# Optimization experiments

Measured on AMD Instinct MI355X. Metric: run time of the kernel, lower is better.

Reference implementation:

```python
import jax, jax.numpy as jnp
import numpy as np

I1, I2, N = 256, 256, 512
B = 2048
FLAT = (I1 + 1) * (I2 + 1)  # 66049


def setup_inputs() -> dict:
    key = jax.random.key(0)
    k1, k2, k3, k4 = jax.random.split(key, 4)
    s1 = 1.0 / np.sqrt(FLAT)
    s2 = 1.0 / np.sqrt(N)
    return {
        "inp1": jax.random.normal(k1, (B, I1), dtype=jnp.float32),
        "inp2": jax.random.normal(k2, (B, I2), dtype=jnp.float32),
        "W1": jax.random.normal(k3, (FLAT, N), dtype=jnp.float32) * s1,
        "b1": jnp.zeros((N,), dtype=jnp.float32),
        "W2": jax.random.normal(k4, (N, N), dtype=jnp.float32) * s2,
        "b2": jnp.zeros((N,), dtype=jnp.float32),
    }


def reference(inp1, inp2, W1, b1, W2, b2):
    b = inp1.shape[0]
    ones = jnp.ones((b, 1), dtype=inp1.dtype)
    a = jnp.concatenate([inp1, ones], axis=-1)  # [B, I1+1]
    c = jnp.concatenate([inp2, ones], axis=-1)  # [B, I2+1]
    # per-sample outer product, flattened: [B, (I1+1)*(I2+1)]
    fusion = jnp.einsum("bi,bj->bij", a, c).reshape(b, -1)
    h = jax.nn.relu(fusion @ W1 + b1)
    return jax.nn.relu(h @ W2 + b2)
```

## Files before the change

### kernel.cpp

```cpp
#include <hip/hip_runtime.h>
#include <hip/hip_bf16.h>
#include <stdint.h>

#define BATCH 2048
#define NHID  512
#define KMAIN 65792
#define KPAD  66112
#define NSTEP 1033
#define SPLITS 8
#define AW 320
#define CW 256

typedef __attribute__((ext_vector_type(8))) short short8;
typedef __attribute__((ext_vector_type(4))) short short4v;
typedef __attribute__((ext_vector_type(4))) float f32x4;

#define AS1 __attribute__((address_space(1)))
#define AS3 __attribute__((address_space(3)))

__device__ __forceinline__ unsigned short f2bf(float f) {
    union { float f; unsigned int u; } v; v.f = f;
    unsigned int r = v.u + 0x7FFFu + ((v.u >> 16) & 1u);
    return (unsigned short)(r >> 16);
}
__device__ __forceinline__ float bf2f(unsigned short u) {
    union { unsigned int i; float f; } v; v.i = ((unsigned int)u) << 16;
    return v.f;
}

__device__ __forceinline__ int w1_src_row(int k) {
    if (k < KMAIN) return (k >> 8) * 257 + (k & 255);
    int i = k - KMAIN;
    return (i < 257) ? (i * 257 + 256) : -1;
}

__global__ __launch_bounds__(256) void prep_kernel(
        const float* __restrict__ inp1, const float* __restrict__ inp2,
        const float* __restrict__ W1, const float* __restrict__ W2,
        unsigned short* __restrict__ W1t, unsigned short* __restrict__ W2t,
        unsigned short* __restrict__ a_tab, unsigned short* __restrict__ c_tab) {
    __shared__ float T[64][65];
    int b = blockIdx.x;
    int t = threadIdx.x;

    if (b < 8264 + 64) {
        const float* src; unsigned short* dst; int k0, n0, Kpad; bool perm;
        if (b < 8264) {
            int kt = b % 1033, nt = b / 1033;
            src = W1; dst = W1t; k0 = kt * 64; n0 = nt * 64; Kpad = KPAD; perm = true;
        } else {
            int bb = b - 8264;
            int kt = bb & 7, nt = bb >> 3;
            src = W2; dst = W2t; k0 = kt * 64; n0 = nt * 64; Kpad = 512; perm = false;
        }
        int nn = t & 63, kk0 = t >> 6;
#pragma unroll
        for (int it = 0; it < 16; ++it) {
            int kk = it * 4 + kk0;
            int k = k0 + kk;
            int row = perm ? w1_src_row(k) : k;
            float v = (row >= 0) ? src[(long)row * NHID + n0 + nn] : 0.f;
            T[kk][nn] = v;
        }
        __syncthreads();
#pragma unroll
        for (int it = 0; it < 2; ++it) {
            int idx = it * 256 + t;
            int nl = idx >> 3, ch = idx & 7;
            short8 o;
#pragma unroll
            for (int e = 0; e < 8; ++e) o[e] = (short)f2bf(T[ch * 8 + e][nl]);
            *reinterpret_cast<short8*>(&dst[(long)(n0 + nl) * Kpad + k0 + ch * 8]) = o;
        }
    } else {
        int r0 = (b - 8328) * 32;
        for (int idx = t; idx < 32 * (AW / 8); idx += 256) {
            int r = idx / 40, ch = idx - r * 40;
            int m = r0 + r;
            short8 o;
#pragma unroll
            for (int e = 0; e < 8; ++e) {
                int i = ch * 8 + e;
                float v = (i < 256) ? inp1[m * 256 + i] : (i == 256 ? 1.0f : 0.0f);
                o[e] = (short)f2bf(v);
            }
            *reinterpret_cast<short8*>(&a_tab[m * AW + ch * 8]) = o;
        }
        for (int idx = t; idx < 32 * (CW / 8); idx += 256) {
            int r = idx >> 5, ch = idx & 31;
            int m = r0 + r;
            short8 o;
#pragma unroll
            for (int e = 0; e < 8; ++e) o[e] = (short)f2bf(inp2[m * 256 + ch * 8 + e]);
            *reinterpret_cast<short8*>(&c_tab[m * CW + ch * 8]) = o;
        }
    }
}

__device__ __forceinline__ void stage_tile128(const unsigned short* __restrict__ g,
        long row0, long k0, long ld, unsigned short* lds) {
    int t = threadIdx.x;
    int wave = t >> 6, lane = t & 63;
    int rl = lane >> 3;
    int ch = (lane & 7) ^ rl;
    const unsigned short* src0 = g + (row0 + wave * 8 + rl) * ld + k0 + ch * 8;
#pragma unroll
    for (int r = 0; r < 4; ++r) {
        const unsigned short* src = src0 + (long)r * 32 * ld;
        unsigned short* dst = lds + (r * 32 + wave * 8) * 64;
        __builtin_amdgcn_global_load_lds((const AS1 unsigned int*)src,
                                         (AS3 unsigned int*)dst, 16, 0, 0);
    }
}

__device__ __forceinline__ short8 read_frag(const unsigned short* lds,
        int rowbase, int kofs, int lane) {
    int row = rowbase + (lane & 15);
    int chunkL = (kofs >> 3) + (lane >> 4);
    int sw = chunkL ^ (row & 7);
    return *reinterpret_cast<const short8*>(&lds[row * 64 + sw * 8]);
}

__global__ __launch_bounds__(256, 2) void gemm1_kernel(
        const unsigned short* __restrict__ a_tab,
        const unsigned short* __restrict__ c_tab,
        const unsigned short* __restrict__ W1t, float* __restrict__ hacc) {
    __shared__ __align__(16) unsigned short B_s[3 * 128 * 64];
    __shared__ __align__(16) unsigned short a_lds[128 * 40];

    int bid = (blockIdx.x & 7) * 64 + (blockIdx.x >> 3);
    int m0 = (bid & 15) * 128;
    int n0 = ((bid >> 4) & 3) * 128;
    int s  = bid >> 6;
    int st0 = s * 128;
    int stLast = st0 + 127;

    int lane = threadIdx.x & 63;
    int wv = threadIdx.x >> 6;
    int lrow = wv * 32 + (lane & 15);
    int rowA0g = m0 + lrow;
    int rowA1g = rowA0g + 16;
    int kq = (lane >> 4) * 8;
    int r4 = (lane >> 4) * 4;
    int abase = wv * 32 + r4;

    short8 cc0[8], cc1[8];
#pragma unroll
    for (int q = 0; q < 8; ++q) {
        cc0[q] = *reinterpret_cast<const short8*>(&c_tab[rowA0g * CW + kq + q * 32]);
        cc1[q] = *reinterpret_cast<const short8*>(&c_tab[rowA1g * CW + kq + q * 32]);
    }
    for (int u = threadIdx.x; u < 512; u += 256) {
        int r = u >> 2, chk = u & 3;
        short8 v = *reinterpret_cast<const short8*>(&a_tab[(m0 + r) * AW + s * 32 + chk * 8]);
        *reinterpret_cast<short8*>(&a_lds[r * 40 + chk * 8]) = v;
    }

    f32x4 acc[2][8];
#pragma unroll
    for (int a = 0; a < 2; ++a)
#pragma unroll
        for (int b = 0; b < 8; ++b) acc[a][b] = (f32x4){0.f, 0.f, 0.f, 0.f};

    stage_tile128(W1t, n0, (long)st0 * 64, KPAD, B_s);
    stage_tile128(W1t, n0, (long)(st0 + 1) * 64, KPAD, B_s + 8192);
    __syncthreads();

    int cur = 0;
    for (int g = 0; g < 32; ++g) {
        f32x4 P[2][8];
#pragma unroll
        for (int a = 0; a < 2; ++a)
#pragma unroll
            for (int b = 0; b < 8; ++b) P[a][b] = (f32x4){0.f, 0.f, 0.f, 0.f};
#pragma unroll
        for (int p = 0; p < 4; ++p) {
            int st = st0 + g * 4 + p;
            if (st == stLast) asm volatile("s_waitcnt vmcnt(0)" ::: "memory");
            else              asm volatile("s_waitcnt vmcnt(4)" ::: "memory");
            __builtin_amdgcn_s_barrier();
            __builtin_amdgcn_sched_barrier(0);
            if (st + 2 <= stLast) {
                int nb = cur + 2; if (nb >= 3) nb -= 3;
                stage_tile128(W1t, n0, (long)(st + 2) * 64, KPAD, B_s + nb * 8192);
            }
            const unsigned short* bb = B_s + cur * 8192;
            __builtin_amdgcn_s_setprio(1);
#pragma unroll
            for (int kk = 0; kk < 2; ++kk) {
                short8 aA = cc0[2 * p + kk];
                short8 aB = cc1[2 * p + kk];
#pragma unroll
                for (int fn = 0; fn < 8; ++fn) {
                    short8 bF = read_frag(bb, fn * 16, kk * 32, lane);
                    P[0][fn] = __builtin_amdgcn_mfma_f32_16x16x32_bf16(
                        aA, bF, P[0][fn], 0, 0, 0);
                    P[1][fn] = __builtin_amdgcn_mfma_f32_16x16x32_bf16(
                        aB, bF, P[1][fn], 0, 0, 0);
                }
            }
            __builtin_amdgcn_s_setprio(0);
            cur = (cur == 2) ? 0 : cur + 1;
        }
        float avA[4], avB[4];
#pragma unroll
        for (int r = 0; r < 4; ++r) {
            avA[r] = bf2f(a_lds[(abase + r) * 40 + g]);
            avB[r] = bf2f(a_lds[(abase + 16 + r) * 40 + g]);
        }
#pragma unroll
        for (int fn = 0; fn < 8; ++fn)
#pragma unroll
            for (int r = 0; r < 4; ++r) {
                acc[0][fn][r] += avA[r] * P[0][fn][r];
                acc[1][fn][r] += avB[r] * P[1][fn][r];
            }
    }

    if (s == 7) {
#pragma unroll
        for (int p = 0; p < 4; ++p) {
            __syncthreads();
            stage_tile128(W1t, n0, (long)(1024 + p) * 64, KPAD, B_s);
            __syncthreads();
#pragma unroll
            for (int kk = 0; kk < 2; ++kk) {
                short8 aA = cc0[2 * p + kk];
                short8 aB = cc1[2 * p + kk];
#pragma unroll
                for (int fn = 0; fn < 8; ++fn) {
                    short8 bF = read_frag(B_s, fn * 16, kk * 32, lane);
                    acc[0][fn] = __builtin_amdgcn_mfma_f32_16x16x32_bf16(
                        aA, bF, acc[0][fn], 0, 0, 0);
                    acc[1][fn] = __builtin_amdgcn_mfma_f32_16x16x32_bf16(
                        aB, bF, acc[1][fn], 0, 0, 0);
                }
            }
        }
        for (int st = 1028; st < 1033; ++st) {
            __syncthreads();
            stage_tile128(W1t, n0, (long)st * 64, KPAD, B_s);
            int koff = (st - 1028) * 64 + kq;
            short8 t00 = *reinterpret_cast<const short8*>(&a_tab[rowA0g * AW + koff]);
            short8 t01 = *reinterpret_cast<const short8*>(&a_tab[rowA0g * AW + koff + 32]);
            short8 t10 = *reinterpret_cast<const short8*>(&a_tab[rowA1g * AW + koff]);
            short8 t11 = *reinterpret_cast<const short8*>(&a_tab[rowA1g * AW + koff + 32]);
            __syncthreads();
#pragma unroll
            for (int kk = 0; kk < 2; ++kk) {
                short8 aA = kk ? t01 : t00;
                short8 aB = kk ? t11 : t10;
#pragma unroll
                for (int fn = 0; fn < 8; ++fn) {
                    short8 bF = read_frag(B_s, fn * 16, kk * 32, lane);
                    acc[0][fn] = __builtin_amdgcn_mfma_f32_16x16x32_bf16(
                        aA, bF, acc[0][fn], 0, 0, 0);
                    acc[1][fn] = __builtin_amdgcn_mfma_f32_16x16x32_bf16(
                        aB, bF, acc[1][fn], 0, 0, 0);
                }
            }
        }
    }

    int cl = lane & 15;
#pragma unroll
    for (int fm = 0; fm < 2; ++fm)
#pragma unroll
        for (int fn = 0; fn < 8; ++fn)
#pragma unroll
            for (int r = 0; r < 4; ++r) {
                int row = m0 + wv * 32 + fm * 16 + r4 + r;
                int col = n0 + fn * 16 + cl;
                atomicAdd(&hacc[row * NHID + col], acc[fm][fn][r]);
            }
}

__global__ __launch_bounds__(256) void bias_relu_h_kernel(
        const float* __restrict__ hacc, const float* __restrict__ b1,
        unsigned short* __restrict__ h) {
    int idx = blockIdx.x * 256 + threadIdx.x;
    f32x4 v = ((const f32x4*)hacc)[idx];
    int col = (idx & 127) << 2;
    f32x4 bb = *(const f32x4*)(b1 + col);
    short4v o;
#pragma unroll
    for (int e = 0; e < 4; ++e) {
        float x = v[e] + bb[e];
        x = fmaxf(x, 0.f);
        o[e] = (short)f2bf(x);
    }
    ((short4v*)h)[idx] = o;
}

__global__ __launch_bounds__(256) void gemm2_kernel(
        const unsigned short* __restrict__ h, const unsigned short* __restrict__ W2t,
        const float* __restrict__ b2, float* __restrict__ out) {
    __shared__ unsigned short A_s[128 * 64];
    __shared__ unsigned short B_s[128 * 64];
    int m0 = (blockIdx.x >> 2) * 128;
    int n0 = (blockIdx.x & 3) * 128;
    int lane = threadIdx.x & 63;
    int wv = threadIdx.x >> 6;
    int wm = (wv >> 1) * 64;
    int wn = (wv & 1) * 64;

    f32x4 acc[4][4];
#pragma unroll
    for (int a = 0; a < 4; ++a)
#pragma unroll
        for (int b = 0; b < 4; ++b) acc[a][b] = (f32x4){0.f, 0.f, 0.f, 0.f};

    for (int st = 0; st < 8; ++st) {
        int kbase = st * 64;
        __syncthreads();
        stage_tile128(h,   m0, kbase, NHID, A_s);
        stage_tile128(W2t, n0, kbase, NHID, B_s);
        __syncthreads();
#pragma unroll
        for (int kk = 0; kk < 2; ++kk) {
            short8 aF[4], bF[4];
#pragma unroll
            for (int fm = 0; fm < 4; ++fm) aF[fm] = read_frag(A_s, wm + fm * 16, kk * 32, lane);
#pragma unroll
            for (int fn = 0; fn < 4; ++fn) bF[fn] = read_frag(B_s, wn + fn * 16, kk * 32, lane);
#pragma unroll
            for (int fm = 0; fm < 4; ++fm)
#pragma unroll
                for (int fn = 0; fn < 4; ++fn)
                    acc[fm][fn] = __builtin_amdgcn_mfma_f32_16x16x32_bf16(
                        aF[fm], bF[fn], acc[fm][fn], 0, 0, 0);
        }
    }
    int cl = lane & 15;
    int r4 = (lane >> 4) * 4;
#pragma unroll
    for (int fm = 0; fm < 4; ++fm)
#pragma unroll
        for (int fn = 0; fn < 4; ++fn)
#pragma unroll
            for (int r = 0; r < 4; ++r) {
                int row = m0 + wm + fm * 16 + r4 + r;
                int col = n0 + wn + fn * 16 + cl;
                float x = acc[fm][fn][r] + b2[col];
                out[row * NHID + col] = fmaxf(x, 0.f);
            }
}

extern "C" void kernel_launch(void* const* d_in, const int* in_sizes, int n_in,
                              void* d_out, int out_size, void* d_ws, size_t ws_size,
                              hipStream_t stream) {
    const float* inp1 = (const float*)d_in[0];
    const float* inp2 = (const float*)d_in[1];
    const float* W1   = (const float*)d_in[2];
    const float* b1   = (const float*)d_in[3];
    const float* W2   = (const float*)d_in[4];
    const float* b2   = (const float*)d_in[5];
    float* out = (float*)d_out;

    size_t off = 0;
    auto alloc = [&](size_t bytes) {
        void* p = (char*)d_ws + off;
        off += (bytes + 255) & ~(size_t)255;
        return p;
    };
    unsigned short* W1t   = (unsigned short*)alloc((size_t)NHID * KPAD * 2);
    unsigned short* W2t   = (unsigned short*)alloc((size_t)NHID * NHID * 2);
    unsigned short* h     = (unsigned short*)alloc((size_t)BATCH * NHID * 2);
    unsigned short* a_tab = (unsigned short*)alloc((size_t)BATCH * AW * 2);
    unsigned short* c_tab = (unsigned short*)alloc((size_t)BATCH * CW * 2);
    (void)ws_size; (void)in_sizes; (void)n_in; (void)out_size;

    hipMemsetAsync(d_out, 0, (size_t)BATCH * NHID * 4, stream);

    prep_kernel<<<8264 + 64 + 64, 256, 0, stream>>>(inp1, inp2, W1, W2,
                                                    W1t, W2t, a_tab, c_tab);

    gemm1_kernel<<<16 * 4 * SPLITS, 256, 0, stream>>>(a_tab, c_tab, W1t, (float*)d_out);
    bias_relu_h_kernel<<<(BATCH * NHID / 4) / 256, 256, 0, stream>>>((const float*)d_out, b1, h);
    gemm2_kernel<<<64, 256, 0, stream>>>(h, W2t, b2, out);
}
```

Measured before the change: 209.3 us.

## Retile gemm1 to 64-row blocks with 4 K-splits and per-wave N slices

Changes the gemm1 tiling from 128x128 tiles with 8 K-splits to 64x128 tiles with 4 K-splits. Each wave now owns a 32-column N slice and all 64 M rows, so it reads only two B fragments per k-step instead of eight. The a-scalars are stored transposed in LDS so one vector load fetches four of them. The aim is less LDS fragment traffic per MFMA and fewer split-K atomics. The cost is that each B tile staged from W1t is reused across only 64 rows, so total W1 reads from global memory double.

```diff
diff --git a/kernel.cpp b/kernel.cpp
--- a/kernel.cpp
+++ b/kernel.cpp
@@ -7,7 +7,7 @@
 #define KMAIN 65792
 #define KPAD  66112
 #define NSTEP 1033
-#define SPLITS 8
+#define SPLITS 4
 #define AW 320
 #define CW 256
 
@@ -126,53 +126,53 @@
         const unsigned short* __restrict__ c_tab,
         const unsigned short* __restrict__ W1t, float* __restrict__ hacc) {
     __shared__ __align__(16) unsigned short B_s[3 * 128 * 64];
-    __shared__ __align__(16) unsigned short a_lds[128 * 40];
+    __shared__ __align__(16) unsigned short a_ldsT[64 * 64];
 
     int bid = (blockIdx.x & 7) * 64 + (blockIdx.x >> 3);
-    int m0 = (bid & 15) * 128;
-    int n0 = ((bid >> 4) & 3) * 128;
-    int s  = bid >> 6;
-    int st0 = s * 128;
-    int stLast = st0 + 127;
+    int m0 = (bid & 31) * 64;
+    int n0 = ((bid >> 5) & 3) * 128;
+    int s  = bid >> 7;
+    int st0 = s * 256;
+    int stLast = st0 + 255;
 
     int lane = threadIdx.x & 63;
     int wv = threadIdx.x >> 6;
-    int lrow = wv * 32 + (lane & 15);
-    int rowA0g = m0 + lrow;
-    int rowA1g = rowA0g + 16;
+    int frow = lane & 15;
     int kq = (lane >> 4) * 8;
     int r4 = (lane >> 4) * 4;
-    int abase = wv * 32 + r4;
-
-    short8 cc0[8], cc1[8];
-#pragma unroll
-    for (int q = 0; q < 8; ++q) {
-        cc0[q] = *reinterpret_cast<const short8*>(&c_tab[rowA0g * CW + kq + q * 32]);
-        cc1[q] = *reinterpret_cast<const short8*>(&c_tab[rowA1g * CW + kq + q * 32]);
-    }
-    for (int u = threadIdx.x; u < 512; u += 256) {
-        int r = u >> 2, chk = u & 3;
-        short8 v = *reinterpret_cast<const short8*>(&a_tab[(m0 + r) * AW + s * 32 + chk * 8]);
-        *reinterpret_cast<short8*>(&a_lds[r * 40 + chk * 8]) = v;
-    }
-
-    f32x4 acc[2][8];
-#pragma unroll
-    for (int a = 0; a < 2; ++a)
-#pragma unroll
-        for (int b = 0; b < 8; ++b) acc[a][b] = (f32x4){0.f, 0.f, 0.f, 0.f};
+
+    short8 cc[4][8];
+#pragma unroll
+    for (int fm = 0; fm < 4; ++fm)
+#pragma unroll
+        for (int q = 0; q < 8; ++q)
+            cc[fm][q] = *reinterpret_cast<const short8*>(
+                &c_tab[(m0 + fm * 16 + frow) * CW + kq + q * 32]);
+
+#pragma unroll
+    for (int e = 0; e < 16; ++e) {
+        int idx = threadIdx.x * 16 + e;
+        int i = idx >> 6, row = idx & 63;
+        a_ldsT[idx] = a_tab[(m0 + row) * AW + s * 64 + i];
+    }
+
+    f32x4 acc[4][2];
+#pragma unroll
+    for (int a = 0; a < 4; ++a)
+#pragma unroll
+        for (int b = 0; b < 2; ++b) acc[a][b] = (f32x4){0.f, 0.f, 0.f, 0.f};
 
     stage_tile128(W1t, n0, (long)st0 * 64, KPAD, B_s);
     stage_tile128(W1t, n0, (long)(st0 + 1) * 64, KPAD, B_s + 8192);
     __syncthreads();
 
     int cur = 0;
-    for (int g = 0; g < 32; ++g) {
-        f32x4 P[2][8];
-#pragma unroll
-        for (int a = 0; a < 2; ++a)
-#pragma unroll
-            for (int b = 0; b < 8; ++b) P[a][b] = (f32x4){0.f, 0.f, 0.f, 0.f};
+    for (int g = 0; g < 64; ++g) {
+        f32x4 P[4][2];
+#pragma unroll
+        for (int a = 0; a < 4; ++a)
+#pragma unroll
+            for (int b = 0; b < 2; ++b) P[a][b] = (f32x4){0.f, 0.f, 0.f, 0.f};
 #pragma unroll
         for (int p = 0; p < 4; ++p) {
             int st = st0 + g * 4 + p;
@@ -188,36 +188,32 @@
             __builtin_amdgcn_s_setprio(1);
 #pragma unroll
             for (int kk = 0; kk < 2; ++kk) {
-                short8 aA = cc0[2 * p + kk];
-                short8 aB = cc1[2 * p + kk];
-#pragma unroll
-                for (int fn = 0; fn < 8; ++fn) {
-                    short8 bF = read_frag(bb, fn * 16, kk * 32, lane);
-                    P[0][fn] = __builtin_amdgcn_mfma_f32_16x16x32_bf16(
-                        aA, bF, P[0][fn], 0, 0, 0);
-                    P[1][fn] = __builtin_amdgcn_mfma_f32_16x16x32_bf16(
-                        aB, bF, P[1][fn], 0, 0, 0);
+                short8 bF0 = read_frag(bb, wv * 32,      kk * 32, lane);
+                short8 bF1 = read_frag(bb, wv * 32 + 16, kk * 32, lane);
+#pragma unroll
+                for (int fm = 0; fm < 4; ++fm) {
+                    P[fm][0] = __builtin_amdgcn_mfma_f32_16x16x32_bf16(
+                        cc[fm][2 * p + kk], bF0, P[fm][0], 0, 0, 0);
+                    P[fm][1] = __builtin_amdgcn_mfma_f32_16x16x32_bf16(
+                        cc[fm][2 * p + kk], bF1, P[fm][1], 0, 0, 0);
                 }
             }
             __builtin_amdgcn_s_setprio(0);
             cur = (cur == 2) ? 0 : cur + 1;
         }
-        float avA[4], avB[4];
-#pragma unroll
-        for (int r = 0; r < 4; ++r) {
-            avA[r] = bf2f(a_lds[(abase + r) * 40 + g]);
-            avB[r] = bf2f(a_lds[(abase + 16 + r) * 40 + g]);
-        }
-#pragma unroll
-        for (int fn = 0; fn < 8; ++fn)
+#pragma unroll
+        for (int fm = 0; fm < 4; ++fm) {
+            short4v a4 = *reinterpret_cast<const short4v*>(&a_ldsT[g * 64 + fm * 16 + r4]);
 #pragma unroll
             for (int r = 0; r < 4; ++r) {
-                acc[0][fn][r] += avA[r] * P[0][fn][r];
-                acc[1][fn][r] += avB[r] * P[1][fn][r];
-            }
-    }
-
-    if (s == 7) {
+                float av = bf2f((unsigned short)a4[r]);
+                acc[fm][0][r] += av * P[fm][0][r];
+                acc[fm][1][r] += av * P[fm][1][r];
+            }
+        }
+    }
+
+    if (s == 3) {
 #pragma unroll
         for (int p = 0; p < 4; ++p) {
             __syncthreads();
@@ -225,15 +221,14 @@
             __syncthreads();
 #pragma unroll
             for (int kk = 0; kk < 2; ++kk) {
-                short8 aA = cc0[2 * p + kk];
-                short8 aB = cc1[2 * p + kk];
-#pragma unroll
-                for (int fn = 0; fn < 8; ++fn) {
-                    short8 bF = read_frag(B_s, fn * 16, kk * 32, lane);
-                    acc[0][fn] = __builtin_amdgcn_mfma_f32_16x16x32_bf16(
-                        aA, bF, acc[0][fn], 0, 0, 0);
-                    acc[1][fn] = __builtin_amdgcn_mfma_f32_16x16x32_bf16(
-                        aB, bF, acc[1][fn], 0, 0, 0);
+                short8 bF0 = read_frag(B_s, wv * 32,      kk * 32, lane);
+                short8 bF1 = read_frag(B_s, wv * 32 + 16, kk * 32, lane);
+#pragma unroll
+                for (int fm = 0; fm < 4; ++fm) {
+                    acc[fm][0] = __builtin_amdgcn_mfma_f32_16x16x32_bf16(
+                        cc[fm][2 * p + kk], bF0, acc[fm][0], 0, 0, 0);
+                    acc[fm][1] = __builtin_amdgcn_mfma_f32_16x16x32_bf16(
+                        cc[fm][2 * p + kk], bF1, acc[fm][1], 0, 0, 0);
                 }
             }
         }
@@ -241,36 +236,37 @@
             __syncthreads();
             stage_tile128(W1t, n0, (long)st * 64, KPAD, B_s);
             int koff = (st - 1028) * 64 + kq;
-            short8 t00 = *reinterpret_cast<const short8*>(&a_tab[rowA0g * AW + koff]);
-            short8 t01 = *reinterpret_cast<const short8*>(&a_tab[rowA0g * AW + koff + 32]);
-            short8 t10 = *reinterpret_cast<const short8*>(&a_tab[rowA1g * AW + koff]);
-            short8 t11 = *reinterpret_cast<const short8*>(&a_tab[rowA1g * AW + koff + 32]);
+            short8 tA[4][2];
+#pragma unroll
+            for (int fm = 0; fm < 4; ++fm)
+#pragma unroll
+                for (int kk = 0; kk < 2; ++kk)
+                    tA[fm][kk] = *reinterpret_cast<const short8*>(
+                        &a_tab[(m0 + fm * 16 + frow) * AW + koff + kk * 32]);
             __syncthreads();
 #pragma unroll
             for (int kk = 0; kk < 2; ++kk) {
-                short8 aA = kk ? t01 : t00;
-                short8 aB = kk ? t11 : t10;
-#pragma unroll
-                for (int fn = 0; fn < 8; ++fn) {
-                    short8 bF = read_frag(B_s, fn * 16, kk * 32, lane);
-                    acc[0][fn] = __builtin_amdgcn_mfma_f32_16x16x32_bf16(
-                        aA, bF, acc[0][fn], 0, 0, 0);
-                    acc[1][fn] = __builtin_amdgcn_mfma_f32_16x16x32_bf16(
-                        aB, bF, acc[1][fn], 0, 0, 0);
+                short8 bF0 = read_frag(B_s, wv * 32,      kk * 32, lane);
+                short8 bF1 = read_frag(B_s, wv * 32 + 16, kk * 32, lane);
+#pragma unroll
+                for (int fm = 0; fm < 4; ++fm) {
+                    acc[fm][0] = __builtin_amdgcn_mfma_f32_16x16x32_bf16(
+                        tA[fm][kk], bF0, acc[fm][0], 0, 0, 0);
+                    acc[fm][1] = __builtin_amdgcn_mfma_f32_16x16x32_bf16(
+                        tA[fm][kk], bF1, acc[fm][1], 0, 0, 0);
                 }
             }
         }
     }
 
-    int cl = lane & 15;
-#pragma unroll
-    for (int fm = 0; fm < 2; ++fm)
-#pragma unroll
-        for (int fn = 0; fn < 8; ++fn)
+#pragma unroll
+    for (int fm = 0; fm < 4; ++fm)
+#pragma unroll
+        for (int fn = 0; fn < 2; ++fn)
 #pragma unroll
             for (int r = 0; r < 4; ++r) {
-                int row = m0 + wv * 32 + fm * 16 + r4 + r;
-                int col = n0 + fn * 16 + cl;
+                int row = m0 + fm * 16 + r4 + r;
+                int col = n0 + wv * 32 + fn * 16 + frow;
                 atomicAdd(&hacc[row * NHID + col], acc[fm][fn][r]);
             }
 }
@@ -375,7 +371,7 @@
     prep_kernel<<<8264 + 64 + 64, 256, 0, stream>>>(inp1, inp2, W1, W2,
                                                     W1t, W2t, a_tab, c_tab);
 
-    gemm1_kernel<<<16 * 4 * SPLITS, 256, 0, stream>>>(a_tab, c_tab, W1t, (float*)d_out);
+    gemm1_kernel<<<32 * 4 * SPLITS, 256, 0, stream>>>(a_tab, c_tab, W1t, (float*)d_out);
     bias_relu_h_kernel<<<(BATCH * NHID / 4) / 256, 256, 0, stream>>>((const float*)d_out, b1, h);
     gemm2_kernel<<<64, 256, 0, stream>>>(h, W2t, b2, out);
 }
```

New measurement: 258.6 us. +23.5%, slower.
